# Kernel tuning notes

Measured on AMD Instinct MI355X. Metric: run time of the kernel, lower is better.

The kernel has to match this reference:

```python
import jax, jax.numpy as jnp
import numpy as np

K = 256
L = 1.0 / K
W = L / 2.5


def setup_inputs() -> dict:
    key = jax.random.key(0)
    x = jax.random.uniform(key, (8, 512, 512), dtype=jnp.float32)
    return {"x": x}


def reference(x) -> jnp.ndarray:
    B, H, Wd = x.shape
    N = H * Wd
    mu_k = (L * (jnp.arange(K, dtype=x.dtype) + 0.5))  # [K]
    xf = x.reshape(B, 1, N)                             # [B,1,N]
    d = xf - mu_k[None, :, None]                        # [B,K,N]
    pj = jax.nn.sigmoid((d + L / 2) / W) - jax.nn.sigmoid((d - L / 2) / W)
    return pj.sum(axis=2) / N                           # [B,K]
```

## Files before the change

### kernel.cpp

```cpp
#include <hip/hip_runtime.h>
#include <hip/hip_bf16.h>


constexpr int KBINS   = 256;
constexpr int FSUB    = 16;
constexpr int LPAD    = 64;
constexpr int TAPS    = 145;
constexpr int LDS_FH  = 4360;
constexpr int NPB     = 512 * 512;
constexpr int BLK_PER_BATCH = 32;
constexpr int CHUNK   = NPB / BLK_PER_BATCH;
constexpr int THREADS = 1024;

__device__ __forceinline__ int skew(int p) { return p + (p >> 5); }

__global__ __launch_bounds__(THREADS)
void hist_kernel(const float* __restrict__ x, float* __restrict__ out) {
    __shared__ unsigned fh[LDS_FH];
    __shared__ float w[TAPS];
    const int tid = threadIdx.x;

    for (int i = tid; i < LDS_FH; i += THREADS) fh[i] = 0u;

    if (tid < TAPS) {
        float a = 0.15625f * (float)(tid - 64);
        float b = 0.15625f * (float)(tid - 80);
        w[tid] = 1.f / (1.f + __expf(-a)) - 1.f / (1.f + __expf(-b));
    }
    __syncthreads();

    const int b     = blockIdx.x / BLK_PER_BATCH;
    const int chunk = blockIdx.x % BLK_PER_BATCH;
    const float4* xv = (const float4*)(x + (size_t)b * NPB + (size_t)chunk * CHUNK);

    #pragma unroll
    for (int it = 0; it < CHUNK / (4 * THREADS); ++it) {
        float4 v = xv[it * THREADS + tid];
        float vals[4] = {v.x, v.y, v.z, v.w};
        int addr[4];
        #pragma unroll
        for (int c = 0; c < 4; ++c) {
            float s = fmaf(vals[c], (float)(KBINS * FSUB), (float)LPAD + 0.5f);
            s = fminf(fmaxf(s, 0.f), 4224.f);
            addr[c] = skew((int)s);
        }
        #pragma unroll
        for (int c = 0; c < 4; ++c)
            atomicAdd(&fh[addr[c]], 1u);
    }
    __syncthreads();

    {
        const int bin = tid >> 2;
        const int q   = tid & 3;
        const int j0  = q * 37;
        const int j1  = (j0 + 37 < TAPS) ? j0 + 37 : TAPS;
        const int base = bin * FSUB;
        float acc = 0.f;
        #pragma unroll 4
        for (int j = j0; j < j1; ++j)
            acc += w[j] * (float)fh[skew(base + j)];
        acc += __shfl_xor(acc, 1);
        acc += __shfl_xor(acc, 2);
        if (q == 0)
            unsafeAtomicAdd(&out[b * KBINS + bin], acc * (1.f / (float)NPB));
    }
}

extern "C" void kernel_launch(void* const* d_in, const int* in_sizes, int n_in,
                              void* d_out, int out_size, void* d_ws, size_t ws_size,
                              hipStream_t stream) {
    const float* x = (const float*)d_in[0];
    float* out = (float*)d_out;
    const int B = in_sizes[0] / NPB;

    hipMemsetAsync(d_out, 0, (size_t)out_size * sizeof(float), stream);
    hist_kernel<<<B * BLK_PER_BATCH, THREADS, 0, stream>>>(x, out);
}
```

Baseline: 60.05 us.

## Split histogram atomics between LDS and global memory, add separate reduce kernel

Half of each thread's four samples now go to a per-batch global-memory fine histogram using global atomics, and the other half stay on the LDS histogram. The aim is to relieve contention on LDS atomics by sending part of the traffic to L2 atomics. Per-block partial results are written to a workspace instead of being atomically added to the output. A second kernel convolves the global histogram with the taps and sums the block partials. This adds a kernel launch, a workspace memset, and contended global atomics on the same bins across 32 blocks per batch.

Result: slower. 108.3 us (+80.4%).

```diff
diff --git a/kernel.cpp b/kernel.cpp
--- a/kernel.cpp
+++ b/kernel.cpp
@@ -11,11 +11,13 @@
 constexpr int BLK_PER_BATCH = 32;
 constexpr int CHUNK   = NPB / BLK_PER_BATCH;
 constexpr int THREADS = 1024;
+constexpr int GH_STRIDE = 4352;
 
 __device__ __forceinline__ int skew(int p) { return p + (p >> 5); }
 
 __global__ __launch_bounds__(THREADS)
-void hist_kernel(const float* __restrict__ x, float* __restrict__ out) {
+void hist_kernel(const float* __restrict__ x, unsigned* __restrict__ gh,
+                 float* __restrict__ partials) {
     __shared__ unsigned fh[LDS_FH];
     __shared__ float w[TAPS];
     const int tid = threadIdx.x;
@@ -32,21 +34,23 @@
     const int b     = blockIdx.x / BLK_PER_BATCH;
     const int chunk = blockIdx.x % BLK_PER_BATCH;
     const float4* xv = (const float4*)(x + (size_t)b * NPB + (size_t)chunk * CHUNK);
+    unsigned* ghb = gh + (size_t)b * GH_STRIDE;
 
     #pragma unroll
     for (int it = 0; it < CHUNK / (4 * THREADS); ++it) {
         float4 v = xv[it * THREADS + tid];
         float vals[4] = {v.x, v.y, v.z, v.w};
-        int addr[4];
+        int p[4];
         #pragma unroll
         for (int c = 0; c < 4; ++c) {
             float s = fmaf(vals[c], (float)(KBINS * FSUB), (float)LPAD + 0.5f);
             s = fminf(fmaxf(s, 0.f), 4224.f);
-            addr[c] = skew((int)s);
+            p[c] = (int)s;
         }
-        #pragma unroll
-        for (int c = 0; c < 4; ++c)
-            atomicAdd(&fh[addr[c]], 1u);
+        atomicAdd(&fh[skew(p[0])], 1u);
+        atomicAdd(&ghb[p[2]], 1u);
+        atomicAdd(&fh[skew(p[1])], 1u);
+        atomicAdd(&ghb[p[3]], 1u);
     }
     __syncthreads();
 
@@ -63,8 +67,35 @@
         acc += __shfl_xor(acc, 1);
         acc += __shfl_xor(acc, 2);
         if (q == 0)
-            unsafeAtomicAdd(&out[b * KBINS + bin], acc * (1.f / (float)NPB));
+            partials[(size_t)blockIdx.x * KBINS + bin] = acc;
     }
+}
+
+__global__ __launch_bounds__(KBINS)
+void reduce_kernel(const unsigned* __restrict__ gh, const float* __restrict__ partials,
+                   float* __restrict__ out) {
+    __shared__ float w[TAPS];
+    const int b = blockIdx.x;
+    const int k = threadIdx.x;
+    if (k < TAPS) {
+        float a = 0.15625f * (float)(k - 64);
+        float c = 0.15625f * (float)(k - 80);
+        w[k] = 1.f / (1.f + __expf(-a)) - 1.f / (1.f + __expf(-c));
+    }
+    __syncthreads();
+
+    float acc = 0.f;
+    const unsigned* g = gh + (size_t)b * GH_STRIDE + k * FSUB;
+    #pragma unroll 8
+    for (int j = 0; j < TAPS; ++j)
+        acc += w[j] * (float)g[j];
+
+    const float* p = partials + (size_t)b * BLK_PER_BATCH * KBINS + k;
+    #pragma unroll
+    for (int c = 0; c < BLK_PER_BATCH; ++c)
+        acc += p[(size_t)c * KBINS];
+
+    out[b * KBINS + k] = acc * (1.f / (float)NPB);
 }
 
 extern "C" void kernel_launch(void* const* d_in, const int* in_sizes, int n_in,
@@ -74,6 +105,10 @@
     float* out = (float*)d_out;
     const int B = in_sizes[0] / NPB;
 
-    hipMemsetAsync(d_out, 0, (size_t)out_size * sizeof(float), stream);
-    hist_kernel<<<B * BLK_PER_BATCH, THREADS, 0, stream>>>(x, out);
+    unsigned* gh = (unsigned*)d_ws;
+    float* partials = (float*)d_ws + (size_t)B * GH_STRIDE;
+
+    hipMemsetAsync(d_ws, 0, (size_t)B * GH_STRIDE * sizeof(unsigned), stream);
+    hist_kernel<<<B * BLK_PER_BATCH, THREADS, 0, stream>>>(x, gh, partials);
+    reduce_kernel<<<B, KBINS, 0, stream>>>(gh, partials, out);
 }
```

## Replace memset and global atomics with partials buffer plus reduce kernel; prefetch inputs early

Applied to the files above, without the earlier changes.

The histogram kernel now issues both float4 loads before clearing LDS and building the weight table, so memory latency overlaps that setup. Each block writes its per-bin partial sums to a workspace buffer instead of doing float atomics into the output. A second small kernel sums the 32 partials per batch and scales them, which removes the hipMemsetAsync. This trades the memset and the atomics for an extra kernel launch and a workspace round trip, and it relies on the workspace being large enough.

New measurement: 60.87 us. Within noise of the previous version (+1.4%).

```diff
diff --git a/kernel.cpp b/kernel.cpp
--- a/kernel.cpp
+++ b/kernel.cpp
@@ -15,37 +15,37 @@
 __device__ __forceinline__ int skew(int p) { return p + (p >> 5); }
 
 __global__ __launch_bounds__(THREADS)
-void hist_kernel(const float* __restrict__ x, float* __restrict__ out) {
+void hist_kernel(const float* __restrict__ x, float* __restrict__ partials) {
     __shared__ unsigned fh[LDS_FH];
     __shared__ float w[TAPS];
     const int tid = threadIdx.x;
+
+    const int b     = blockIdx.x / BLK_PER_BATCH;
+    const int chunk = blockIdx.x % BLK_PER_BATCH;
+    const float4* xv = (const float4*)(x + (size_t)b * NPB + (size_t)chunk * CHUNK);
+    const float4 v0 = xv[tid];
+    const float4 v1 = xv[THREADS + tid];
 
     for (int i = tid; i < LDS_FH; i += THREADS) fh[i] = 0u;
 
     if (tid < TAPS) {
         float a = 0.15625f * (float)(tid - 64);
-        float b = 0.15625f * (float)(tid - 80);
-        w[tid] = 1.f / (1.f + __expf(-a)) - 1.f / (1.f + __expf(-b));
+        float c = 0.15625f * (float)(tid - 80);
+        w[tid] = 1.f / (1.f + __expf(-a)) - 1.f / (1.f + __expf(-c));
     }
     __syncthreads();
 
-    const int b     = blockIdx.x / BLK_PER_BATCH;
-    const int chunk = blockIdx.x % BLK_PER_BATCH;
-    const float4* xv = (const float4*)(x + (size_t)b * NPB + (size_t)chunk * CHUNK);
-
-    #pragma unroll
-    for (int it = 0; it < CHUNK / (4 * THREADS); ++it) {
-        float4 v = xv[it * THREADS + tid];
-        float vals[4] = {v.x, v.y, v.z, v.w};
-        int addr[4];
+    {
+        const float vals[8] = {v0.x, v0.y, v0.z, v0.w, v1.x, v1.y, v1.z, v1.w};
+        int addr[8];
         #pragma unroll
-        for (int c = 0; c < 4; ++c) {
+        for (int c = 0; c < 8; ++c) {
             float s = fmaf(vals[c], (float)(KBINS * FSUB), (float)LPAD + 0.5f);
             s = fminf(fmaxf(s, 0.f), 4224.f);
             addr[c] = skew((int)s);
         }
         #pragma unroll
-        for (int c = 0; c < 4; ++c)
+        for (int c = 0; c < 8; ++c)
             atomicAdd(&fh[addr[c]], 1u);
     }
     __syncthreads();
@@ -63,8 +63,25 @@
         acc += __shfl_xor(acc, 1);
         acc += __shfl_xor(acc, 2);
         if (q == 0)
-            unsafeAtomicAdd(&out[b * KBINS + bin], acc * (1.f / (float)NPB));
+            partials[(size_t)blockIdx.x * KBINS + bin] = acc;
     }
+}
+
+__global__ __launch_bounds__(THREADS)
+void reduce_kernel(const float* __restrict__ partials, float* __restrict__ out) {
+    const int b   = blockIdx.x;
+    const int tid = threadIdx.x;
+    const int bin = tid >> 2;
+    const int q   = tid & 3;
+    const float* p = partials + (size_t)b * BLK_PER_BATCH * KBINS + bin;
+    float s = 0.f;
+    #pragma unroll
+    for (int i = 0; i < 8; ++i)
+        s += p[(size_t)(q * 8 + i) * KBINS];
+    s += __shfl_xor(s, 1);
+    s += __shfl_xor(s, 2);
+    if (q == 0)
+        out[b * KBINS + bin] = s * (1.f / (float)NPB);
 }
 
 extern "C" void kernel_launch(void* const* d_in, const int* in_sizes, int n_in,
@@ -72,8 +89,9 @@
                               hipStream_t stream) {
     const float* x = (const float*)d_in[0];
     float* out = (float*)d_out;
+    float* partials = (float*)d_ws;
     const int B = in_sizes[0] / NPB;
 
-    hipMemsetAsync(d_out, 0, (size_t)out_size * sizeof(float), stream);
-    hist_kernel<<<B * BLK_PER_BATCH, THREADS, 0, stream>>>(x, out);
+    hist_kernel<<<B * BLK_PER_BATCH, THREADS, 0, stream>>>(x, partials);
+    reduce_kernel<<<B, THREADS, 0, stream>>>(partials, out);
 }
```
